# Optimization experiments

Hardware: AMD Instinct MI355X
Metric: run time of the kernel (lower is better)

Reference implementation:

```python
import jax, jax.numpy as jnp
import numpy as np
import math

D_MODEL, D_STATE, D_CONV = 1024, 16, 4
D_INNER = 2 * D_MODEL
DT_RANK = math.ceil(D_MODEL / 16)
B, L = 4, 2048


def setup_inputs() -> dict:
    key = jax.random.key(0)
    ks = jax.random.split(key, 10)
    s = 0.02
    x = jax.random.normal(ks[0], (B, L, D_MODEL), dtype=jnp.float32)
    ln_g = jnp.ones((D_MODEL,), jnp.float32)
    ln_b = jnp.zeros((D_MODEL,), jnp.float32)
    W_in = jax.random.normal(ks[1], (D_MODEL, 2 * D_INNER), jnp.float32) * s
    conv_w = jax.random.normal(ks[2], (D_INNER, 1, D_CONV), jnp.float32) * s
    conv_b = jnp.zeros((D_INNER,), jnp.float32)
    W_xp = jax.random.normal(ks[3], (D_INNER, DT_RANK + 2 * D_STATE), jnp.float32) * s
    W_dt = jax.random.normal(ks[4], (DT_RANK, D_INNER), jnp.float32) * (DT_RANK ** -0.5)
    # inverse-softplus of dt ~ 0.01 (between dt_min=0.001 and dt_max=0.1)
    dt_bias = jnp.full((D_INNER,), float(np.log(np.expm1(0.01))), jnp.float32)
    # S4D-real init: A = 1..d_state per channel
    A_log = jnp.log(jnp.broadcast_to(jnp.arange(1, D_STATE + 1, dtype=jnp.float32), (D_INNER, D_STATE)))
    D_skip = jnp.ones((D_INNER,), jnp.float32)
    W_out = jax.random.normal(ks[5], (D_INNER, D_MODEL), jnp.float32) * s
    return dict(x=x, ln_g=ln_g, ln_b=ln_b, W_in=W_in, conv_w=conv_w, conv_b=conv_b,
                W_xp=W_xp, W_dt=W_dt, dt_bias=dt_bias, A_log=A_log, D_skip=D_skip, W_out=W_out)


def _layernorm(x, g, b, eps=1e-5):
    m = jnp.mean(x, axis=-1, keepdims=True)
    v = jnp.mean(jnp.square(x - m), axis=-1, keepdims=True)
    return (x - m) * jax.lax.rsqrt(v + eps) * g + b


def _mamba(xn, W_in, conv_w, conv_b, W_xp, W_dt, dt_bias, A_log, D_skip, W_out):
    # xn: [B, L, d_model]
    xz = xn @ W_in                                   # [B, L, 2*d_inner]
    xi, z = jnp.split(xz, 2, axis=-1)                # each [B, L, d_inner]
    # depthwise causal conv over sequence
    xi_t = jnp.transpose(xi, (0, 2, 1))              # [B, d_inner, L]
    xc = jax.lax.conv_general_dilated(
        xi_t, conv_w, window_strides=(1,), padding=[(D_CONV - 1, 0)],
        feature_group_count=D_INNER, dimension_numbers=('NCH', 'OIH', 'NCH'))
    xc = jnp.transpose(xc, (0, 2, 1)) + conv_b       # [B, L, d_inner]
    xc = jax.nn.silu(xc)
    # input-dependent dt, B, C
    x_dbl = xc @ W_xp                                # [B, L, dt_rank + 2*d_state]
    dt_lo, Bm, Cm = jnp.split(x_dbl, [DT_RANK, DT_RANK + D_STATE], axis=-1)
    delta = jax.nn.softplus(dt_lo @ W_dt + dt_bias)  # [B, L, d_inner]
    A = -jnp.exp(A_log)                              # [d_inner, d_state]

    def step(h, inp):
        dt_t, B_t, C_t, u_t = inp                    # [B,D], [B,N], [B,N], [B,D]
        dA = jnp.exp(dt_t[..., None] * A)            # [B, D, N]
        h = h * dA + (dt_t * u_t)[..., None] * B_t[:, None, :]
        y = jnp.einsum('bdn,bn->bd', h, C_t)
        return h, y

    h0 = jnp.zeros((xn.shape[0], D_INNER, D_STATE), xn.dtype)
    inputs = (jnp.transpose(delta, (1, 0, 2)), jnp.transpose(Bm, (1, 0, 2)),
              jnp.transpose(Cm, (1, 0, 2)), jnp.transpose(xc, (1, 0, 2)))
    _, ys = jax.lax.scan(step, h0, inputs)           # ys: [L, B, d_inner]
    y = jnp.transpose(ys, (1, 0, 2)) + xc * D_skip   # [B, L, d_inner]
    y = y * jax.nn.silu(z)
    return y @ W_out                                 # [B, L, d_model]


def reference(x, ln_g, ln_b, W_in, conv_w, conv_b, W_xp, W_dt, dt_bias, A_log, D_skip, W_out):
    xn = _layernorm(x, ln_g, ln_b)
    return _mamba(xn, W_in, conv_w, conv_b, W_xp, W_dt, dt_bias, A_log, D_skip, W_out) + x
```

## Files before the change

### kernel.cpp

```cpp
#include <hip/hip_runtime.h>

#define DM 1024
#define DI 2048
#define DS 16
#define DTR 64
#define LL 2048
#define NROW 8192

typedef unsigned short u16;
typedef unsigned int u32;
typedef __bf16 bf16x8 __attribute__((ext_vector_type(8)));
typedef float f32x4 __attribute__((ext_vector_type(4)));
typedef float v2f __attribute__((ext_vector_type(2)));

__device__ __forceinline__ float bf2f(u16 u) {
  unsigned int v = ((unsigned int)u) << 16;
  return __builtin_bit_cast(float, v);
}
__device__ __forceinline__ u16 f2bf(float f) {
  unsigned int x = __builtin_bit_cast(unsigned int, f);
  x = x + 0x7fffu + ((x >> 16) & 1u);
  return (u16)(x >> 16);
}
__device__ __forceinline__ float lo_bf(u32 v) { return __builtin_bit_cast(float, v << 16); }
__device__ __forceinline__ float hi_bf(u32 v) { return __builtin_bit_cast(float, v & 0xFFFF0000u); }
__device__ __forceinline__ u32 pack_bf(float a, float b) {
  return (u32)f2bf(a) | ((u32)f2bf(b) << 16);
}
__device__ __forceinline__ bool io_f32(const u16* lng) { return lng[0] == 0; }

__device__ __forceinline__ void async16(const void* g, void* l) {
  __builtin_amdgcn_global_load_lds(
      (const __attribute__((address_space(1))) unsigned int*)g,
      (__attribute__((address_space(3))) unsigned int*)l, 16, 0, 0);
}

__device__ __forceinline__ void pow16v(float e1, v2f* E) {
  float e2 = e1 * e1;
  v2f sq = {e2, e2};
  E[0] = (v2f){e1, e2};
#pragma unroll
  for (int k = 1; k < 8; k++) E[k] = E[k - 1] * sq;
}

__device__ void transpose_dev(const void* __restrict__ in, u16* __restrict__ out,
                              int R, int C, int Cp, int bx, int by, bool f32,
                              int tid, u16 (*tile)[33]) {
  int c0 = bx * 32, r0 = by * 32;
  int tx = tid & 31, ty = tid >> 5;
#pragma unroll
  for (int i = 0; i < 4; i++) {
    int r = r0 + ty + i * 8, c = c0 + tx;
    u16 v = 0;
    if (r < R && c < C) {
      if (f32) v = f2bf(((const float*)in)[(size_t)r * C + c]);
      else     v = ((const u16*)in)[(size_t)r * C + c];
    }
    tile[ty + i * 8][tx] = v;
  }
  __syncthreads();
#pragma unroll
  for (int i = 0; i < 4; i++) {
    int oc = c0 + ty + i * 8, orr = r0 + tx;
    if (oc < Cp && orr < R) out[(size_t)oc * R + orr] = tile[tx][ty + i * 8];
  }
}

__global__ __launch_bounds__(256) void prep_k(
    const void* __restrict__ W_in, u16* __restrict__ W_inT,
    const void* __restrict__ W_dt, u16* __restrict__ W_dtT,
    const void* __restrict__ W_xp, u16* __restrict__ W_xpT,
    const void* __restrict__ W_out, u16* __restrict__ W_outT,
    const void* __restrict__ x, const u16* __restrict__ g,
    const u16* __restrict__ b, u16* __restrict__ xn) {
  __shared__ u16 tile[32][33];
  __shared__ float rs_[4], rq_[4];
  bool f32 = io_f32(g);
  int tid = threadIdx.x;
  int bid = blockIdx.x;
  if (bid < 4096) {
    transpose_dev(W_in, W_inT, 1024, 4096, 4096, bid & 127, bid >> 7, f32, tid, tile);
    return;
  } else if (bid < 4224) {
    bid -= 4096;
    transpose_dev(W_dt, W_dtT, 64, 2048, 2048, bid & 63, bid >> 6, f32, tid, tile);
    return;
  } else if (bid < 4480) {
    bid -= 4224;
    transpose_dev(W_xp, W_xpT, 2048, 96, 128, bid & 3, bid >> 2, f32, tid, tile);
    return;
  } else if (bid < 6528) {
    bid -= 4480;
    transpose_dev(W_out, W_outT, 2048, 1024, 1024, bid & 31, bid >> 5, f32, tid, tile);
    return;
  }
  int row = bid - 6528;
  float f[4];
  if (f32) {
    float4 v = ((const float4*)((const float*)x + (size_t)row * DM))[tid];
    f[0] = v.x; f[1] = v.y; f[2] = v.z; f[3] = v.w;
  } else {
    ushort4 v = ((const ushort4*)((const u16*)x + (size_t)row * DM))[tid];
    f[0] = bf2f(v.x); f[1] = bf2f(v.y); f[2] = bf2f(v.z); f[3] = bf2f(v.w);
  }
  float s = f[0] + f[1] + f[2] + f[3];
  float q = f[0] * f[0] + f[1] * f[1] + f[2] * f[2] + f[3] * f[3];
#pragma unroll
  for (int off = 32; off; off >>= 1) {
    s += __shfl_down(s, off, 64);
    q += __shfl_down(q, off, 64);
  }
  int wid = tid >> 6, lane = tid & 63;
  if (lane == 0) { rs_[wid] = s; rq_[wid] = q; }
  __syncthreads();
  float ts = rs_[0] + rs_[1] + rs_[2] + rs_[3];
  float tq = rq_[0] + rq_[1] + rq_[2] + rq_[3];
  float mean = ts * (1.f / DM);
  float var = tq * (1.f / DM) - mean * mean;
  float inv = rsqrtf(var + 1e-5f);
  int c = tid * 4;
  ushort4 o;
  u16* po = (u16*)&o;
#pragma unroll
  for (int k = 0; k < 4; k++) {
    float gk = f32 ? ((const float*)g)[c + k] : bf2f(g[c + k]);
    float bk = f32 ? ((const float*)b)[c + k] : bf2f(b[c + k]);
    po[k] = f2bf((f[k] - mean) * inv * gk + bk);
  }
  ((ushort4*)(xn + (size_t)row * DM))[tid] = o;
}

template <int EPI>
__device__ __forceinline__ void gemm_body(const u16* __restrict__ A,
                                          const u16* __restrict__ BT,
                                          void* __restrict__ C,
                                          const void* __restrict__ extra,
                                          int M, int N, int Klen, int ldk,
                                          const u16* __restrict__ lng, int mOff,
                                          u16* ldsA, u16* ldsB) {
  int tid = threadIdx.x;
  int wid = tid >> 6, lane = tid & 63;
  int l15 = lane & 15, quad = lane >> 4;
  int bm = blockIdx.x * 128;
  int bn;
  const u16* Ae = A;
  const u16* Be = BT;
  float* Cpart = nullptr;
  if (EPI == 5) {
    bn = 0;
    int ky = blockIdx.y;
    Ae += (size_t)ky * Klen;
    Be += (size_t)ky * Klen;
    Cpart = (float*)C + (size_t)ky * M * N;
  } else {
    bn = blockIdx.y * 128;
  }
  int wrow = (wid >> 1) * 64, wcol = (wid & 1) * 64;

  f32x4 zero = {0.f, 0.f, 0.f, 0.f};
  f32x4 acc[4][4];
#pragma unroll
  for (int i = 0; i < 4; i++)
#pragma unroll
    for (int j = 0; j < 4; j++) acc[i][j] = zero;

  int row0 = tid >> 2;
  int colb = (tid & 3) * 16;
  const char* Ap0 = (const char*)Ae + ((size_t)(bm + row0) * ldk) * 2 + colb;
  const char* Ap1 = (const char*)Ae + ((size_t)(bm + row0 + 64) * ldk) * 2 + colb;
  const char* Bp0 = (const char*)Be + ((size_t)(bn + row0) * ldk) * 2 + colb;
  const char* Bp1 = (const char*)Be + ((size_t)(bn + row0 + 64) * ldk) * 2 + colb;
  u16* la = ldsA + wid * 512;
  u16* lb = ldsB + wid * 512;

  for (int k0 = 0; k0 < Klen; k0 += 64) {
    size_t kb = (size_t)k0 * 2;
    async16(Ap0 + kb, la);
    async16(Ap1 + kb, la + 2048);
    async16(Ap0 + kb + 64, la + 4096);
    async16(Ap1 + kb + 64, la + 6144);
    async16(Bp0 + kb, lb);
    async16(Bp1 + kb, lb + 2048);
    async16(Bp0 + kb + 64, lb + 4096);
    async16(Bp1 + kb + 64, lb + 6144);
    __syncthreads();
#pragma unroll
    for (int s = 0; s < 2; s++) {
      bf16x8 af[4], bfr[4];
#pragma unroll
      for (int i = 0; i < 4; i++)
        af[i] = *(const bf16x8*)&ldsA[s * 4096 + (wrow + i * 16 + l15) * 32 + quad * 8];
#pragma unroll
      for (int j = 0; j < 4; j++)
        bfr[j] = *(const bf16x8*)&ldsB[s * 4096 + (wcol + j * 16 + l15) * 32 + quad * 8];
#pragma unroll
      for (int i = 0; i < 4; i++)
#pragma unroll
        for (int j = 0; j < 4; j++)
          acc[i][j] = __builtin_amdgcn_mfma_f32_16x16x32_bf16(af[i], bfr[j], acc[i][j], 0, 0, 0);
    }
    __syncthreads();
  }

  bool f32 = (EPI == 2 || EPI == 3) ? io_f32(lng) : false;
  if ((EPI == 2 || EPI == 3) && !f32) {
    u16* tile = ldsA;
#pragma unroll
    for (int i = 0; i < 4; i++) {
#pragma unroll
      for (int j = 0; j < 4; j++) {
        int gn = bn + wcol + j * 16 + l15;
#pragma unroll
        for (int r = 0; r < 4; r++) {
          int lr = wrow + i * 16 + quad * 4 + r;
          float v = acc[i][j][r];
          if (EPI == 2) {
            v += bf2f(((const u16*)extra)[gn]);
            v = (v > 20.f) ? v : log1pf(__expf(v));
          } else {
            v += bf2f(((const u16*)extra)[(size_t)(bm + lr + mOff) * N + gn]);
          }
          tile[lr * 128 + wcol + j * 16 + l15] = f2bf(v);
        }
      }
    }
    __syncthreads();
#pragma unroll
    for (int g = 0; g < 8; g++) {
      int gi = g * 256 + tid;
      int row = gi >> 4, cg = gi & 15;
      uint4 v4 = *(const uint4*)&tile[row * 128 + cg * 8];
      *(uint4*)((u16*)C + (size_t)(bm + row + mOff) * N + bn + cg * 8) = v4;
    }
    return;
  }
#pragma unroll
  for (int i = 0; i < 4; i++) {
#pragma unroll
    for (int j = 0; j < 4; j++) {
      int gn = bn + wcol + j * 16 + l15;
#pragma unroll
      for (int r = 0; r < 4; r++) {
        int gm = bm + wrow + i * 16 + quad * 4 + r;
        float v = acc[i][j][r];
        if (EPI == 2) {
          float bias = ((const float*)extra)[gn];
          v += bias;
          float sp = (v > 20.f) ? v : log1pf(__expf(v));
          ((u16*)C)[(size_t)gm * N + gn] = f2bf(sp);
        } else if (EPI == 3) {
          size_t idx = (size_t)(gm + mOff) * N + gn;
          v += ((const float*)extra)[idx];
          ((float*)C)[idx] = v;
        } else {
          Cpart[(size_t)gm * N + gn] = v;
        }
      }
    }
  }
}

#define GEMM_WRAP(name, EPI)                                                        \
  __global__ __launch_bounds__(256) void name(                                      \
      const u16* __restrict__ A, const u16* __restrict__ BT, void* __restrict__ C,  \
      const void* __restrict__ extra, int M, int N, int Klen, int ldk,              \
      const u16* __restrict__ lng, int mOff) {                                      \
    __shared__ __align__(16) u16 lds[16384];                                        \
    gemm_body<EPI>(A, BT, C, extra, M, N, Klen, ldk, lng, mOff, lds, lds + 8192);   \
  }

GEMM_WRAP(gemm_xp_k, 5)
GEMM_WRAP(gemm_dt_k, 2)
GEMM_WRAP(gemm_out_k, 3)

__global__ __launch_bounds__(512, 2) void gemm_in256_k(
    const u16* __restrict__ A, const u16* __restrict__ BT,
    u16* __restrict__ C, u16* __restrict__ Z, int ldk, int Klen) {
  __shared__ __align__(16) u16 lds[65536];
  const int tid = threadIdx.x;
  const int wid = tid >> 6, lane = tid & 63;
  const int l15 = lane & 15, quad = lane >> 4;
  const int bm = blockIdx.x * 256, bn = blockIdx.y * 256;
  const int wrow = (wid >> 2) * 128;
  const int wcol = (wid & 3) * 64;

  const int srow = tid >> 3;
  const int sg = ((tid & 7) ^ (srow & 7)) * 8;
  const u16* Ag[4];
  const u16* Bg[4];
#pragma unroll
  for (int s = 0; s < 4; s++) {
    Ag[s] = A + (size_t)(bm + s * 64 + srow) * ldk + sg;
    Bg[s] = BT + (size_t)(bn + s * 64 + srow) * ldk + sg;
  }
  const int sdst = wid * 512;

  int rA[2], rB[2];
#pragma unroll
  for (int ks = 0; ks < 2; ks++) {
    int gsw = ((ks * 4 + quad) ^ (l15 & 7)) * 8;
    rA[ks] = (wrow + l15) * 64 + gsw;
    rB[ks] = 16384 + (wcol + l15) * 64 + gsw;
  }

  f32x4 acc[8][4];
  f32x4 zero = {0.f, 0.f, 0.f, 0.f};
#pragma unroll
  for (int i = 0; i < 8; i++)
#pragma unroll
    for (int j = 0; j < 4; j++) acc[i][j] = zero;

  const int NT = Klen >> 6;
  async16(Ag[0], &lds[sdst]);
  async16(Ag[1], &lds[4096 + sdst]);
  async16(Ag[2], &lds[8192 + sdst]);
  async16(Ag[3], &lds[12288 + sdst]);
  async16(Bg[0], &lds[16384 + sdst]);
  async16(Bg[1], &lds[20480 + sdst]);
  async16(Bg[2], &lds[24576 + sdst]);
  async16(Bg[3], &lds[28672 + sdst]);
  if (NT > 1) {
    async16(Ag[0] + 64, &lds[32768 + sdst]);
    async16(Ag[1] + 64, &lds[36864 + sdst]);
    async16(Ag[2] + 64, &lds[40960 + sdst]);
    async16(Ag[3] + 64, &lds[45056 + sdst]);
    async16(Bg[0] + 64, &lds[49152 + sdst]);
    async16(Bg[1] + 64, &lds[53248 + sdst]);
    async16(Bg[2] + 64, &lds[57344 + sdst]);
    async16(Bg[3] + 64, &lds[61440 + sdst]);
  }
  asm volatile("s_waitcnt vmcnt(8)" ::: "memory");
  __builtin_amdgcn_s_barrier();
  __builtin_amdgcn_sched_barrier(0);

  bf16x8 aLo[4][2], aHi[4][2], b0[2][2], b1[2][2];
#pragma unroll
  for (int mf = 0; mf < 4; mf++) {
    aLo[mf][0] = *(const bf16x8*)&lds[rA[0] + mf * 1024];
    aLo[mf][1] = *(const bf16x8*)&lds[rA[1] + mf * 1024];
  }
#pragma unroll
  for (int nf = 0; nf < 2; nf++)
#pragma unroll
    for (int ks = 0; ks < 2; ks++) {
      b0[nf][ks] = *(const bf16x8*)&lds[rB[ks] + nf * 1024];
      b1[nf][ks] = *(const bf16x8*)&lds[rB[ks] + (2 + nf) * 1024];
    }

  for (int t = 0; t < NT; ++t) {
    const int bb = (t & 1) << 15;
    const int nb = bb ^ 32768;
    const int k2 = (t + 2) << 6;
    const bool st1 = (t + 1 < NT), st2 = (t + 2 < NT);

    __builtin_amdgcn_s_setprio(1);
#pragma unroll
    for (int ks = 0; ks < 2; ks++)
#pragma unroll
      for (int mf = 0; mf < 4; mf++)
#pragma unroll
        for (int nf = 0; nf < 2; nf++)
          acc[mf][nf] = __builtin_amdgcn_mfma_f32_16x16x32_bf16(aLo[mf][ks], b0[nf][ks], acc[mf][nf], 0, 0, 0);
    __builtin_amdgcn_s_setprio(0);
#pragma unroll
    for (int mf = 0; mf < 4; mf++) {
      aHi[mf][0] = *(const bf16x8*)&lds[bb + rA[0] + 4096 + mf * 1024];
      aHi[mf][1] = *(const bf16x8*)&lds[bb + rA[1] + 4096 + mf * 1024];
    }
    __builtin_amdgcn_s_setprio(1);
#pragma unroll
    for (int ks = 0; ks < 2; ks++)
#pragma unroll
      for (int mf = 0; mf < 4; mf++)
#pragma unroll
        for (int nf = 0; nf < 2; nf++)
          acc[mf][2 + nf] = __builtin_amdgcn_mfma_f32_16x16x32_bf16(aLo[mf][ks], b1[nf][ks], acc[mf][2 + nf], 0, 0, 0);
    __builtin_amdgcn_s_setprio(0);

    asm volatile("s_waitcnt lgkmcnt(0)" ::: "memory");
    __builtin_amdgcn_sched_barrier(0);
    asm volatile("s_waitcnt vmcnt(0)" ::: "memory");
    __builtin_amdgcn_s_barrier();
    __builtin_amdgcn_sched_barrier(0);

    if (st2) {
      async16(Ag[0] + k2, &lds[bb + sdst]);
      async16(Ag[1] + k2, &lds[bb + 4096 + sdst]);
      async16(Ag[2] + k2, &lds[bb + 8192 + sdst]);
      async16(Ag[3] + k2, &lds[bb + 12288 + sdst]);
      async16(Bg[0] + k2, &lds[bb + 16384 + sdst]);
      async16(Bg[1] + k2, &lds[bb + 20480 + sdst]);
      async16(Bg[2] + k2, &lds[bb + 24576 + sdst]);
      async16(Bg[3] + k2, &lds[bb + 28672 + sdst]);
    }
    if (st1) {
#pragma unroll
      for (int mf = 0; mf < 4; mf++) {
        aLo[mf][0] = *(const bf16x8*)&lds[nb + rA[0] + mf * 1024];
        aLo[mf][1] = *(const bf16x8*)&lds[nb + rA[1] + mf * 1024];
      }
    }
    __builtin_amdgcn_s_setprio(1);
#pragma unroll
    for (int ks = 0; ks < 2; ks++)
#pragma unroll
      for (int mf = 0; mf < 4; mf++)
#pragma unroll
        for (int nf = 0; nf < 2; nf++)
          acc[4 + mf][nf] = __builtin_amdgcn_mfma_f32_16x16x32_bf16(aHi[mf][ks], b0[nf][ks], acc[4 + mf][nf], 0, 0, 0);
    __builtin_amdgcn_s_setprio(0);
    if (st1) {
#pragma unroll
      for (int nf = 0; nf < 2; nf++)
#pragma unroll
        for (int ks = 0; ks < 2; ks++)
          b0[nf][ks] = *(const bf16x8*)&lds[nb + rB[ks] + nf * 1024];
    }
    __builtin_amdgcn_s_setprio(1);
#pragma unroll
    for (int ks = 0; ks < 2; ks++)
#pragma unroll
      for (int mf = 0; mf < 4; mf++)
#pragma unroll
        for (int nf = 0; nf < 2; nf++)
          acc[4 + mf][2 + nf] = __builtin_amdgcn_mfma_f32_16x16x32_bf16(aHi[mf][ks], b1[nf][ks], acc[4 + mf][2 + nf], 0, 0, 0);
    __builtin_amdgcn_s_setprio(0);
    if (st1) {
#pragma unroll
      for (int nf = 0; nf < 2; nf++)
#pragma unroll
        for (int ks = 0; ks < 2; ks++)
          b1[nf][ks] = *(const bf16x8*)&lds[nb + rB[ks] + (2 + nf) * 1024];
    }
  }

  __syncthreads();
  {
    const bool isZ = (bn >= DI);
#pragma unroll
    for (int i = 0; i < 8; i++) {
#pragma unroll
      for (int j = 0; j < 4; j++) {
        int lc = wcol + j * 16 + l15;
        int gr = lc >> 3, go = lc & 7;
#pragma unroll
        for (int r = 0; r < 4; r++) {
          int lr = wrow + i * 16 + quad * 4 + r;
          float v = acc[i][j][r];
          if (isZ) v = v / (1.f + __expf(-v));
          int grs = gr ^ ((lr & 7) ^ ((lr >> 3) & 7));
          lds[lr * 256 + grs * 8 + go] = f2bf(v);
        }
      }
    }
    __syncthreads();
    u16* outp = isZ ? (Z + (size_t)bm * DI + (bn - DI)) : (C + (size_t)bm * DI + bn);
#pragma unroll
    for (int g = 0; g < 16; g++) {
      int gi = g * 512 + tid;
      int row = gi >> 5, cg = gi & 31;
      int cgs = cg ^ ((row & 7) ^ ((row >> 3) & 7));
      uint4 v4 = *(const uint4*)&lds[row * 256 + cgs * 8];
      *(uint4*)(outp + (size_t)row * DI + cg * 8) = v4;
    }
  }
}

__global__ __launch_bounds__(256) void conv4_k(const u16* __restrict__ xi,
                                               const void* __restrict__ cw,
                                               const void* __restrict__ cb,
                                               u16* __restrict__ xc,
                                               const u16* __restrict__ lng) {
  bool f32 = io_f32(lng);
  int idx = blockIdx.x * 256 + threadIdx.x;
  int c = idx & (DI - 1);
  int rq = idx >> 11;
  int l4 = (rq & (LL / 4 - 1)) * 4;
  int b = rq >> 9;
  float w[4], bias;
  if (f32) {
    float4 w4 = *(const float4*)((const float*)cw + (size_t)c * 4);
    w[0] = w4.x; w[1] = w4.y; w[2] = w4.z; w[3] = w4.w;
    bias = ((const float*)cb)[c];
  } else {
    ushort4 w4 = *(const ushort4*)((const u16*)cw + (size_t)c * 4);
    w[0] = bf2f(w4.x); w[1] = bf2f(w4.y); w[2] = bf2f(w4.z); w[3] = bf2f(w4.w);
    bias = bf2f(((const u16*)cb)[c]);
  }
  size_t base = ((size_t)(b * LL + l4)) * DI + c;
  float v[7];
#pragma unroll
  for (int j = 0; j < 7; j++) {
    int lj = l4 - 3 + j;
    v[j] = (lj >= 0) ? bf2f(xi[base + (size_t)(j - 3) * DI]) : 0.f;
  }
#pragma unroll
  for (int r = 0; r < 4; r++) {
    float acc = bias + v[r] * w[0] + v[r + 1] * w[1] + v[r + 2] * w[2] + v[r + 3] * w[3];
    float sv = acc / (1.f + __expf(-acc));
    xc[base + (size_t)r * DI] = f2bf(sv);
  }
}

__global__ __launch_bounds__(256) void reduce_dtlo_k(const float* __restrict__ Cpart,
                                                     float* __restrict__ xdbl,
                                                     u16* __restrict__ dtlo, int M) {
  int i = blockIdx.x * 256 + threadIdx.x;
  size_t MN = (size_t)M * 128;
  float v = Cpart[i] + Cpart[MN + i] + Cpart[2 * MN + i] + Cpart[3 * MN + i];
  xdbl[i] = v;
  int j = i & 127, m = i >> 7;
  if (j < 64) dtlo[(size_t)m * 64 + j] = f2bf(v);
}

__device__ __forceinline__ bool fastA(const void* A_log, bool f32, int d0) {
  bool fast = true;
#pragma unroll
  for (int c = 0; c < 2; c++)
    for (int n = 0; n < 16; n++) {
      float al = f32 ? ((const float*)A_log)[(d0 + c) * DS + n]
                     : bf2f(((const u16*)A_log)[(d0 + c) * DS + n]);
      float Av = __expf(al);
      fast = fast && (__builtin_fabsf(Av - (float)(n + 1)) <= 1e-3f * (n + 1));
    }
  return fast;
}

template <int S>
__global__ __launch_bounds__(256) void scan_p1(const u16* __restrict__ delta,
                                               const u16* __restrict__ xc,
                                               const float* __restrict__ xdbl,
                                               const void* __restrict__ A_log,
                                               const u16* __restrict__ lng,
                                               float* __restrict__ Pbuf,
                                               float* __restrict__ Lbuf,
                                               float* __restrict__ sumbuf,
                                               int NS) {
  bool f32 = io_f32(lng);
  int tid = threadIdx.x;
  int seg = blockIdx.x, dch = blockIdx.y, bL = blockIdx.z;
  int d0 = (dch * 256 + tid) * 2;
  size_t rb = (size_t)bL * LL;
  int l0 = seg * S;
  extern __shared__ float bc[];
#pragma unroll 2
  for (int i = tid; i < S * 4; i += 256) {
    int t = i >> 2, k = (i & 3) * 4;
    *(float4*)&bc[t * 16 + k] = *(const float4*)&xdbl[(rb + l0 + t) * 128 + 64 + k];
  }
  __syncthreads();
  size_t sb = ((((size_t)bL * NS + seg) * DI) + d0) * DS;
  const u32* dpu = (const u32*)(delta + (rb + l0) * DI + d0);
  const u32* upu = (const u32*)(xc + (rb + l0) * DI + d0);
  if (fastA(A_log, f32, d0)) {
    v2f h0[8], h1[8];
#pragma unroll
    for (int k = 0; k < 8; k++) { h0[k] = (v2f){0.f, 0.f}; h1[k] = (v2f){0.f, 0.f}; }
    float sum0 = 0.f, sum1 = 0.f;
    const int T = 8;
    for (int t0 = 0; t0 < S; t0 += T) {
      u32 dv[T], uv[T];
#pragma unroll
      for (int j = 0; j < T; j++) {
        dv[j] = dpu[j * (DI / 2)];
        uv[j] = upu[j * (DI / 2)];
      }
      dpu += T * (DI / 2);
      upu += T * (DI / 2);
#pragma unroll
      for (int j = 0; j < T; j++) {
        float dt0 = lo_bf(dv[j]), dt1 = hi_bf(dv[j]);
        float u0 = lo_bf(uv[j]), u1 = hi_bf(uv[j]);
        sum0 += dt0; sum1 += dt1;
        const v2f* B2 = (const v2f*)&bc[(t0 + j) * 16];
        v2f E[8];
        pow16v(__expf(-dt0), E);
        float com0 = dt0 * u0;
        v2f cv0 = {com0, com0};
#pragma unroll
        for (int k = 0; k < 8; k++) h0[k] = h0[k] * E[k] + B2[k] * cv0;
        pow16v(__expf(-dt1), E);
        float com1 = dt1 * u1;
        v2f cv1 = {com1, com1};
#pragma unroll
        for (int k = 0; k < 8; k++) h1[k] = h1[k] * E[k] + B2[k] * cv1;
      }
    }
#pragma unroll
    for (int k = 0; k < 8; k++) { *(v2f*)&Lbuf[sb + 2 * k] = h0[k]; *(v2f*)&Lbuf[sb + 16 + 2 * k] = h1[k]; }
    if (sumbuf) {
      *(v2f*)&sumbuf[((size_t)(bL * NS + seg)) * DI + d0] = (v2f){sum0, sum1};
    } else {
      v2f P[8];
      pow16v(__expf(-sum0), P);
#pragma unroll
      for (int k = 0; k < 8; k++) *(v2f*)&Pbuf[sb + 2 * k] = P[k];
      pow16v(__expf(-sum1), P);
#pragma unroll
      for (int k = 0; k < 8; k++) *(v2f*)&Pbuf[sb + 16 + 2 * k] = P[k];
    }
  } else {
    for (int c = 0; c < 2; c++) {
      int d = d0 + c;
      float A2[16], h[16], P[16];
#pragma unroll
      for (int n = 0; n < 16; n++) {
        float al = f32 ? ((const float*)A_log)[d * DS + n] : bf2f(((const u16*)A_log)[d * DS + n]);
        A2[n] = -__expf(al);
        h[n] = 0.f; P[n] = 1.f;
      }
      const u16* dp = delta + (rb + l0) * DI + d;
      const u16* up = xc + (rb + l0) * DI + d;
      for (int t = 0; t < S; t++) {
        float dt = bf2f(dp[(size_t)t * DI]);
        float u = bf2f(up[(size_t)t * DI]);
        float com = dt * u;
        const float* Bf = &bc[t * 16];
#pragma unroll
        for (int n = 0; n < 16; n++) {
          float dA = __expf(dt * A2[n]);
          h[n] = fmaf(h[n], dA, com * Bf[n]);
          P[n] *= dA;
        }
      }
#pragma unroll
      for (int n = 0; n < 16; n++) { Pbuf[sb + 16 * c + n] = P[n]; Lbuf[sb + 16 * c + n] = h[n]; }
    }
  }
}

__global__ __launch_bounds__(256) void scan_p2(float* __restrict__ Pbuf,
                                               float* __restrict__ Lbuf,
                                               const float* __restrict__ sumbuf,
                                               const void* __restrict__ A_log,
                                               const u16* __restrict__ lng, int NS) {
  int idx = blockIdx.x * 256 + threadIdx.x;
  int bL = idx >> 15;
  int dn = idx & 32767;
  int d = dn >> 4, n = dn & 15;
  bool useSum = false;
  if (sumbuf) {
    bool f32 = io_f32(lng);
    useSum = fastA(A_log, f32, d & ~1);
  }
  float np1 = (float)(n + 1);
  float H = 0.f;
  for (int s = 0; s < NS; s++) {
    size_t o = ((size_t)(bL * NS + s) << 15) + dn;
    float Lv = Lbuf[o];
    float P = useSum ? __expf(-sumbuf[((size_t)(bL * NS + s)) * DI + d] * np1)
                     : Pbuf[o];
    Lbuf[o] = H;
    H = fmaf(P, H, Lv);
  }
}

template <int S>
__global__ __launch_bounds__(256) void scan_p3(u16* __restrict__ dy,
                                               const u16* __restrict__ xc,
                                               const float* __restrict__ xdbl,
                                               const u16* __restrict__ z,
                                               const void* __restrict__ A_log,
                                               const void* __restrict__ D_skip,
                                               const u16* __restrict__ lng,
                                               const float* __restrict__ Lbuf,
                                               int NS) {
  bool f32 = io_f32(lng);
  int tid = threadIdx.x;
  int seg = blockIdx.x, dch = blockIdx.y, bL = blockIdx.z;
  int d0 = (dch * 256 + tid) * 2;
  size_t rb = (size_t)bL * LL;
  int l0 = seg * S;
  extern __shared__ float bc[];
#pragma unroll 2
  for (int i = tid; i < S * 8; i += 256) {
    int t = i >> 3, k = (i & 7) * 4;
    *(float4*)&bc[t * 32 + k] = *(const float4*)&xdbl[(rb + l0 + t) * 128 + 64 + k];
  }
  __syncthreads();
  size_t sb = ((((size_t)bL * NS + seg) * DI) + d0) * DS;
  float Dv0 = f32 ? ((const float*)D_skip)[d0] : bf2f(((const u16*)D_skip)[d0]);
  float Dv1 = f32 ? ((const float*)D_skip)[d0 + 1] : bf2f(((const u16*)D_skip)[d0 + 1]);
  u32* dpu = (u32*)(dy + (rb + l0) * DI + d0);
  const u32* upu = (const u32*)(xc + (rb + l0) * DI + d0);
  const u32* zpu = (const u32*)(z + (rb + l0) * DI + d0);
  if (fastA(A_log, f32, d0)) {
    v2f h0[8], h1[8];
#pragma unroll
    for (int k = 0; k < 8; k++) {
      h0[k] = *(const v2f*)&Lbuf[sb + 2 * k];
      h1[k] = *(const v2f*)&Lbuf[sb + 16 + 2 * k];
    }
    const int T = 8;
    for (int t0 = 0; t0 < S; t0 += T) {
      u32 dv[T], uv[T], zv[T];
#pragma unroll
      for (int j = 0; j < T; j++) {
        dv[j] = dpu[j * (DI / 2)];
        uv[j] = upu[j * (DI / 2)];
        zv[j] = zpu[j * (DI / 2)];
      }
      upu += T * (DI / 2);
      zpu += T * (DI / 2);
#pragma unroll
      for (int j = 0; j < T; j++) {
        float dt0 = lo_bf(dv[j]), dt1 = hi_bf(dv[j]);
        float u0 = lo_bf(uv[j]), u1 = hi_bf(uv[j]);
        float zg0 = lo_bf(zv[j]), zg1 = hi_bf(zv[j]);
        const v2f* B2 = (const v2f*)&bc[(t0 + j) * 32];
        const v2f* C2 = (const v2f*)&bc[(t0 + j) * 32 + 16];
        v2f E[8];
        pow16v(__expf(-dt0), E);
        float com0 = dt0 * u0;
        v2f cv = {com0, com0};
        v2f a0 = {0.f, 0.f}, a1 = {0.f, 0.f};
#pragma unroll
        for (int k = 0; k < 8; k += 2) {
          h0[k] = h0[k] * E[k] + B2[k] * cv;
          h0[k + 1] = h0[k + 1] * E[k + 1] + B2[k + 1] * cv;
          a0 += h0[k] * C2[k];
          a1 += h0[k + 1] * C2[k + 1];
        }
        float cs0 = (a0.x + a0.y) + (a1.x + a1.y);
        pow16v(__expf(-dt1), E);
        float com1 = dt1 * u1;
        cv = (v2f){com1, com1};
        a0 = (v2f){0.f, 0.f}; a1 = (v2f){0.f, 0.f};
#pragma unroll
        for (int k = 0; k < 8; k += 2) {
          h1[k] = h1[k] * E[k] + B2[k] * cv;
          h1[k + 1] = h1[k + 1] * E[k + 1] + B2[k + 1] * cv;
          a0 += h1[k] * C2[k];
          a1 += h1[k + 1] * C2[k + 1];
        }
        float cs1 = (a0.x + a0.y) + (a1.x + a1.y);
        float y0 = (cs0 + u0 * Dv0) * zg0;
        float y1 = (cs1 + u1 * Dv1) * zg1;
        dpu[j * (DI / 2)] = pack_bf(y0, y1);
      }
      dpu += T * (DI / 2);
    }
  } else {
    for (int c = 0; c < 2; c++) {
      int d = d0 + c;
      float A2[16], h[16];
#pragma unroll
      for (int n = 0; n < 16; n++) {
        float al = f32 ? ((const float*)A_log)[d * DS + n] : bf2f(((const u16*)A_log)[d * DS + n]);
        A2[n] = -__expf(al);
        h[n] = Lbuf[sb + 16 * c + n];
      }
      float Dv = (c == 0) ? Dv0 : Dv1;
      u16* dp = dy + (rb + l0) * DI + d;
      const u16* up = xc + (rb + l0) * DI + d;
      const u16* zp = z + (rb + l0) * DI + d;
      for (int t = 0; t < S; t++) {
        float dt = bf2f(dp[(size_t)t * DI]);
        float u = bf2f(up[(size_t)t * DI]);
        float zg = bf2f(zp[(size_t)t * DI]);
        float com = dt * u;
        const float* Bf = &bc[t * 32];
        const float* Cf = &bc[t * 32 + 16];
        float cs = 0.f;
#pragma unroll
        for (int n = 0; n < 16; n++) {
          float dA = __expf(dt * A2[n]);
          h[n] = fmaf(h[n], dA, com * Bf[n]);
          cs = fmaf(h[n], Cf[n], cs);
        }
        dp[(size_t)t * DI] = f2bf((cs + u * Dv) * zg);
      }
    }
  }
}

static void launch_scan(int NS, int nb, u16* xi, u16* xc, float* xdbl, u16* z,
                        const u16* A_log, const u16* D_sk, const u16* ln_g,
                        float* Pbuf, float* Lbuf, float* sumbuf,
                        hipStream_t stream) {
  int S = LL / NS;
  dim3 g1(NS, 4, nb);
  if (S == 32) {
    scan_p1<32><<<g1, 256, 32 * 64, stream>>>(xi, xc, xdbl, A_log, ln_g, Pbuf, Lbuf, sumbuf, NS);
  } else if (S == 64) {
    scan_p1<64><<<g1, 256, 64 * 64, stream>>>(xi, xc, xdbl, A_log, ln_g, Pbuf, Lbuf, sumbuf, NS);
  } else {
    scan_p1<128><<<g1, 256, 128 * 64, stream>>>(xi, xc, xdbl, A_log, ln_g, Pbuf, Lbuf, sumbuf, NS);
  }
  scan_p2<<<nb * 128, 256, 0, stream>>>(Pbuf, Lbuf, sumbuf, A_log, ln_g, NS);
  if (S == 32) {
    scan_p3<32><<<g1, 256, 32 * 128, stream>>>(xi, xc, xdbl, z, A_log, D_sk, ln_g, Lbuf, NS);
  } else if (S == 64) {
    scan_p3<64><<<g1, 256, 64 * 128, stream>>>(xi, xc, xdbl, z, A_log, D_sk, ln_g, Lbuf, NS);
  } else {
    scan_p3<128><<<g1, 256, 128 * 128, stream>>>(xi, xc, xdbl, z, A_log, D_sk, ln_g, Lbuf, NS);
  }
}

extern "C" void kernel_launch(void* const* d_in, const int* in_sizes, int n_in,
                              void* d_out, int out_size, void* d_ws, size_t ws_size,
                              hipStream_t stream) {
  const u16* x = (const u16*)d_in[0];
  const u16* ln_g = (const u16*)d_in[1];
  const u16* ln_b = (const u16*)d_in[2];
  const u16* W_in = (const u16*)d_in[3];
  const u16* cw = (const u16*)d_in[4];
  const u16* cb = (const u16*)d_in[5];
  const u16* W_xp = (const u16*)d_in[6];
  const u16* W_dt = (const u16*)d_in[7];
  const u16* dt_b = (const u16*)d_in[8];
  const u16* A_log = (const u16*)d_in[9];
  const u16* D_sk = (const u16*)d_in[10];
  const u16* W_out = (const u16*)d_in[11];

  char* ws = (char*)d_ws;
  const size_t MB = 1024 * 1024;

  if (ws_size >= 124 * MB) {
    int NS = (ws_size >= 180 * MB) ? 64 : (ws_size >= 144 * MB) ? 32 : 16;
    u16* xc = (u16*)(ws + 0);
    u16* xn = xc;
    u16* W_inT = (u16*)(ws + 16 * MB);
    u16* xi = (u16*)(ws + 32 * MB);
    u16* z = (u16*)(ws + 64 * MB);
    float* xdbl = (float*)(ws + 96 * MB);
    u16* dtlo = (u16*)(ws + 100 * MB);
    u16* W_xpT = (u16*)(ws + 101 * MB);
    u16* W_dtT = (u16*)(ws + 102 * MB);
    u16* W_outT = (u16*)(ws + 103 * MB);
    size_t stateSz = (size_t)NS * 4 * DI * DS * 4;
    float* Cpart = (float*)(ws + 107 * MB);
    float* Pbuf = (float*)(ws + 107 * MB);
    float* Lbuf = (float*)(ws + 107 * MB + stateSz);
    float* sumbuf = (NS >= 32) ? (float*)(ws + 107 * MB + 2 * stateSz) : nullptr;

    prep_k<<<6528 + NROW, 256, 0, stream>>>(W_in, W_inT, W_dt, W_dtT, W_xp, W_xpT,
                                            W_out, W_outT, x, ln_g, ln_b, xn);
    gemm_in256_k<<<dim3(NROW / 256, (2 * DI) / 256), 512, 0, stream>>>(xn, W_inT, xi, z, DM, DM);
    conv4_k<<<(NROW / 4 * DI) / 256, 256, 0, stream>>>(xi, cw, cb, xc, ln_g);
    gemm_xp_k<<<dim3(64, 4), 256, 0, stream>>>(xc, W_xpT, Cpart, nullptr, NROW, 128, 512, DI, ln_g, 0);
    reduce_dtlo_k<<<(NROW * 128) / 256, 256, 0, stream>>>(Cpart, xdbl, dtlo, NROW);
    gemm_dt_k<<<dim3(64, 16), 256, 0, stream>>>(dtlo, W_dtT, xi, dt_b, NROW, DI, DTR, DTR, ln_g, 0);
    launch_scan(NS, 4, xi, xc, xdbl, z, A_log, D_sk, ln_g, Pbuf, Lbuf, sumbuf, stream);
    gemm_out_k<<<dim3(64, 8), 256, 0, stream>>>(xi, W_outT, d_out, x, NROW, DM, DI, DI, ln_g, 0);
  } else {
    int NS = 32;
    u16* W_inT = (u16*)(ws + 0);
    u16* W_xpT = (u16*)(ws + 8 * MB);
    u16* W_dtT = (u16*)(ws + 9 * MB);
    u16* W_outT = (u16*)(ws + 10 * MB);
    u16* xn = (u16*)(ws + 14 * MB);
    u16* xi = (u16*)(ws + 30 * MB);
    u16* z = (u16*)(ws + 38 * MB);
    u16* xc = (u16*)(ws + 46 * MB);
    float* xdbl = (float*)(ws + 54 * MB);
    u16* dtlo = (u16*)(ws + 55 * MB);
    float* Cpart = (float*)(ws + 56 * MB);
    float* Pbuf = (float*)(ws + 56 * MB);
    float* Lbuf = (float*)(ws + 61 * MB);

    prep_k<<<6528 + NROW, 256, 0, stream>>>(W_in, W_inT, W_dt, W_dtT, W_xp, W_xpT,
                                            W_out, W_outT, x, ln_g, ln_b, xn);
    for (int b = 0; b < 4; b++) {
      const u16* xnb = xn + (size_t)b * LL * DM;
      gemm_in256_k<<<dim3(LL / 256, (2 * DI) / 256), 512, 0, stream>>>(xnb, W_inT, xi, z, DM, DM);
      conv4_k<<<(LL / 4 * DI) / 256, 256, 0, stream>>>(xi, cw, cb, xc, ln_g);
      gemm_xp_k<<<dim3(16, 4), 256, 0, stream>>>(xc, W_xpT, Cpart, nullptr, LL, 128, 512, DI, ln_g, 0);
      reduce_dtlo_k<<<(LL * 128) / 256, 256, 0, stream>>>(Cpart, xdbl, dtlo, LL);
      gemm_dt_k<<<dim3(16, 16), 256, 0, stream>>>(dtlo, W_dtT, xi, dt_b, LL, DI, DTR, DTR, ln_g, 0);
      launch_scan(NS, 1, xi, xc, xdbl, z, A_log, D_sk, ln_g, Pbuf, Lbuf, nullptr, stream);
      gemm_out_k<<<dim3(16, 8), 256, 0, stream>>>(xi, W_outT, d_out, x, LL, DM, DI, DI, ln_g, b * LL);
    }
  }
}
```

Baseline: 492.6 us.

## Replace output GEMM with 256x128 pipelined kernel and vectorize depthwise conv

Swaps the generic 128x128 output-projection GEMM for a dedicated 512-thread kernel. It uses 256x128 tiles, double-buffered async global-to-LDS loads, swizzled LDS and interleaved MFMA with LDS reads, plus a swizzled bf16 epilogue that adds the residual. The conv kernel now handles 8 channels per thread with 16-byte loads and stores instead of scalar bf16 accesses. The aim is better operand reuse and overlap in the output GEMM and fewer memory transactions in the conv. In exchange, the GEMM uses more LDS and registers per block and gets fewer blocks (256 instead of 512) on the large path.

```diff
diff --git a/kernel.cpp b/kernel.cpp
--- a/kernel.cpp
+++ b/kernel.cpp
@@ -202,8 +202,8 @@
     __syncthreads();
   }
 
-  bool f32 = (EPI == 2 || EPI == 3) ? io_f32(lng) : false;
-  if ((EPI == 2 || EPI == 3) && !f32) {
+  bool f32 = (EPI == 2) ? io_f32(lng) : false;
+  if (EPI == 2 && !f32) {
     u16* tile = ldsA;
 #pragma unroll
     for (int i = 0; i < 4; i++) {
@@ -214,12 +214,8 @@
         for (int r = 0; r < 4; r++) {
           int lr = wrow + i * 16 + quad * 4 + r;
           float v = acc[i][j][r];
-          if (EPI == 2) {
-            v += bf2f(((const u16*)extra)[gn]);
-            v = (v > 20.f) ? v : log1pf(__expf(v));
-          } else {
-            v += bf2f(((const u16*)extra)[(size_t)(bm + lr + mOff) * N + gn]);
-          }
+          v += bf2f(((const u16*)extra)[gn]);
+          v = (v > 20.f) ? v : log1pf(__expf(v));
           tile[lr * 128 + wcol + j * 16 + l15] = f2bf(v);
         }
       }
@@ -248,10 +244,6 @@
           v += bias;
           float sp = (v > 20.f) ? v : log1pf(__expf(v));
           ((u16*)C)[(size_t)gm * N + gn] = f2bf(sp);
-        } else if (EPI == 3) {
-          size_t idx = (size_t)(gm + mOff) * N + gn;
-          v += ((const float*)extra)[idx];
-          ((float*)C)[idx] = v;
         } else {
           Cpart[(size_t)gm * N + gn] = v;
         }
@@ -271,7 +263,6 @@
 
 GEMM_WRAP(gemm_xp_k, 5)
 GEMM_WRAP(gemm_dt_k, 2)
-GEMM_WRAP(gemm_out_k, 3)
 
 __global__ __launch_bounds__(512, 2) void gemm_in256_k(
     const u16* __restrict__ A, const u16* __restrict__ BT,
@@ -466,6 +457,190 @@
   }
 }
 
+__global__ __launch_bounds__(512, 2) void gemm_out256_k(
+    const u16* __restrict__ A, const u16* __restrict__ BT,
+    void* __restrict__ C, const void* __restrict__ extra,
+    int N, int ldk, int Klen, const u16* __restrict__ lng, int mOff) {
+  __shared__ __align__(16) u16 lds[49152];
+  const int tid = threadIdx.x;
+  const int wid = tid >> 6, lane = tid & 63;
+  const int l15 = lane & 15, quad = lane >> 4;
+  const int bm = blockIdx.x * 256, bn = blockIdx.y * 128;
+  const int wrow = (wid >> 2) * 128;
+  const int wcol = (wid & 3) * 32;
+
+  const int srow = tid >> 3;
+  const int sg = ((tid & 7) ^ (srow & 7)) * 8;
+  const u16* Ag[4];
+  const u16* Bg[2];
+#pragma unroll
+  for (int s = 0; s < 4; s++) Ag[s] = A + (size_t)(bm + s * 64 + srow) * ldk + sg;
+#pragma unroll
+  for (int s = 0; s < 2; s++) Bg[s] = BT + (size_t)(bn + s * 64 + srow) * ldk + sg;
+  const int sdst = wid * 512;
+
+  int rA[2], rB[2];
+#pragma unroll
+  for (int ks = 0; ks < 2; ks++) {
+    int gsw = ((ks * 4 + quad) ^ (l15 & 7)) * 8;
+    rA[ks] = (wrow + l15) * 64 + gsw;
+    rB[ks] = 16384 + (wcol + l15) * 64 + gsw;
+  }
+
+  f32x4 acc[8][2];
+  f32x4 zero = {0.f, 0.f, 0.f, 0.f};
+#pragma unroll
+  for (int i = 0; i < 8; i++)
+#pragma unroll
+    for (int j = 0; j < 2; j++) acc[i][j] = zero;
+
+  const int NT = Klen >> 6;
+  async16(Ag[0], &lds[sdst]);
+  async16(Ag[1], &lds[4096 + sdst]);
+  async16(Ag[2], &lds[8192 + sdst]);
+  async16(Ag[3], &lds[12288 + sdst]);
+  async16(Bg[0], &lds[16384 + sdst]);
+  async16(Bg[1], &lds[20480 + sdst]);
+  if (NT > 1) {
+    async16(Ag[0] + 64, &lds[24576 + sdst]);
+    async16(Ag[1] + 64, &lds[24576 + 4096 + sdst]);
+    async16(Ag[2] + 64, &lds[24576 + 8192 + sdst]);
+    async16(Ag[3] + 64, &lds[24576 + 12288 + sdst]);
+    async16(Bg[0] + 64, &lds[24576 + 16384 + sdst]);
+    async16(Bg[1] + 64, &lds[24576 + 20480 + sdst]);
+  }
+  asm volatile("s_waitcnt vmcnt(6)" ::: "memory");
+  __builtin_amdgcn_s_barrier();
+  __builtin_amdgcn_sched_barrier(0);
+
+  bf16x8 aLo[4][2], aHi[4][2], b0[2], b1[2];
+#pragma unroll
+  for (int mf = 0; mf < 4; mf++) {
+    aLo[mf][0] = *(const bf16x8*)&lds[rA[0] + mf * 1024];
+    aLo[mf][1] = *(const bf16x8*)&lds[rA[1] + mf * 1024];
+  }
+#pragma unroll
+  for (int ks = 0; ks < 2; ks++) {
+    b0[ks] = *(const bf16x8*)&lds[rB[ks]];
+    b1[ks] = *(const bf16x8*)&lds[rB[ks] + 1024];
+  }
+
+  for (int t = 0; t < NT; ++t) {
+    const int bb = (t & 1) * 24576;
+    const int nb = bb ^ 24576;
+    const int k2 = (t + 2) << 6;
+    const bool st1 = (t + 1 < NT), st2 = (t + 2 < NT);
+
+    __builtin_amdgcn_s_setprio(1);
+#pragma unroll
+    for (int ks = 0; ks < 2; ks++)
+#pragma unroll
+      for (int mf = 0; mf < 4; mf++)
+        acc[mf][0] = __builtin_amdgcn_mfma_f32_16x16x32_bf16(aLo[mf][ks], b0[ks], acc[mf][0], 0, 0, 0);
+    __builtin_amdgcn_s_setprio(0);
+#pragma unroll
+    for (int mf = 0; mf < 4; mf++) {
+      aHi[mf][0] = *(const bf16x8*)&lds[bb + rA[0] + 4096 + mf * 1024];
+      aHi[mf][1] = *(const bf16x8*)&lds[bb + rA[1] + 4096 + mf * 1024];
+    }
+    __builtin_amdgcn_s_setprio(1);
+#pragma unroll
+    for (int ks = 0; ks < 2; ks++)
+#pragma unroll
+      for (int mf = 0; mf < 4; mf++)
+        acc[mf][1] = __builtin_amdgcn_mfma_f32_16x16x32_bf16(aLo[mf][ks], b1[ks], acc[mf][1], 0, 0, 0);
+    __builtin_amdgcn_s_setprio(0);
+
+    asm volatile("s_waitcnt lgkmcnt(0)" ::: "memory");
+    __builtin_amdgcn_sched_barrier(0);
+    asm volatile("s_waitcnt vmcnt(0)" ::: "memory");
+    __builtin_amdgcn_s_barrier();
+    __builtin_amdgcn_sched_barrier(0);
+
+    if (st2) {
+      async16(Ag[0] + k2, &lds[bb + sdst]);
+      async16(Ag[1] + k2, &lds[bb + 4096 + sdst]);
+      async16(Ag[2] + k2, &lds[bb + 8192 + sdst]);
+      async16(Ag[3] + k2, &lds[bb + 12288 + sdst]);
+      async16(Bg[0] + k2, &lds[bb + 16384 + sdst]);
+      async16(Bg[1] + k2, &lds[bb + 20480 + sdst]);
+    }
+    if (st1) {
+#pragma unroll
+      for (int mf = 0; mf < 4; mf++) {
+        aLo[mf][0] = *(const bf16x8*)&lds[nb + rA[0] + mf * 1024];
+        aLo[mf][1] = *(const bf16x8*)&lds[nb + rA[1] + mf * 1024];
+      }
+    }
+    __builtin_amdgcn_s_setprio(1);
+#pragma unroll
+    for (int ks = 0; ks < 2; ks++)
+#pragma unroll
+      for (int mf = 0; mf < 4; mf++)
+        acc[4 + mf][0] = __builtin_amdgcn_mfma_f32_16x16x32_bf16(aHi[mf][ks], b0[ks], acc[4 + mf][0], 0, 0, 0);
+    __builtin_amdgcn_s_setprio(0);
+    if (st1) {
+#pragma unroll
+      for (int ks = 0; ks < 2; ks++) b0[ks] = *(const bf16x8*)&lds[nb + rB[ks]];
+    }
+    __builtin_amdgcn_s_setprio(1);
+#pragma unroll
+    for (int ks = 0; ks < 2; ks++)
+#pragma unroll
+      for (int mf = 0; mf < 4; mf++)
+        acc[4 + mf][1] = __builtin_amdgcn_mfma_f32_16x16x32_bf16(aHi[mf][ks], b1[ks], acc[4 + mf][1], 0, 0, 0);
+    __builtin_amdgcn_s_setprio(0);
+    if (st1) {
+#pragma unroll
+      for (int ks = 0; ks < 2; ks++) b1[ks] = *(const bf16x8*)&lds[nb + rB[ks] + 1024];
+    }
+  }
+
+  bool f32 = io_f32(lng);
+  __syncthreads();
+  if (!f32) {
+#pragma unroll
+    for (int i = 0; i < 8; i++) {
+#pragma unroll
+      for (int j = 0; j < 2; j++) {
+        int lc = wcol + j * 16 + l15;
+        int gr = lc >> 3, go = lc & 7;
+#pragma unroll
+        for (int r = 0; r < 4; r++) {
+          int lr = wrow + i * 16 + quad * 4 + r;
+          float v = acc[i][j][r];
+          v += bf2f(((const u16*)extra)[(size_t)(bm + lr + mOff) * N + bn + lc]);
+          int grs = gr ^ ((lr & 7) ^ ((lr >> 3) & 7));
+          lds[lr * 128 + grs * 8 + go] = f2bf(v);
+        }
+      }
+    }
+    __syncthreads();
+#pragma unroll
+    for (int g = 0; g < 8; g++) {
+      int gi = g * 512 + tid;
+      int row = gi >> 4, cg = gi & 15;
+      int cgs = cg ^ ((row & 7) ^ ((row >> 3) & 7));
+      uint4 v4 = *(const uint4*)&lds[row * 128 + cgs * 8];
+      *(uint4*)((u16*)C + (size_t)(bm + row + mOff) * N + bn + cg * 8) = v4;
+    }
+  } else {
+#pragma unroll
+    for (int i = 0; i < 8; i++) {
+#pragma unroll
+      for (int j = 0; j < 2; j++) {
+        int gn = bn + wcol + j * 16 + l15;
+#pragma unroll
+        for (int r = 0; r < 4; r++) {
+          int gm = bm + wrow + i * 16 + quad * 4 + r;
+          size_t idx = (size_t)(gm + mOff) * N + gn;
+          ((float*)C)[idx] = acc[i][j][r] + ((const float*)extra)[idx];
+        }
+      }
+    }
+  }
+}
+
 __global__ __launch_bounds__(256) void conv4_k(const u16* __restrict__ xi,
                                                const void* __restrict__ cw,
                                                const void* __restrict__ cb,
@@ -473,32 +648,58 @@
                                                const u16* __restrict__ lng) {
   bool f32 = io_f32(lng);
   int idx = blockIdx.x * 256 + threadIdx.x;
-  int c = idx & (DI - 1);
-  int rq = idx >> 11;
+  int c8 = (idx & (DI / 8 - 1)) * 8;
+  int rq = idx >> 8;
   int l4 = (rq & (LL / 4 - 1)) * 4;
   int b = rq >> 9;
-  float w[4], bias;
-  if (f32) {
-    float4 w4 = *(const float4*)((const float*)cw + (size_t)c * 4);
-    w[0] = w4.x; w[1] = w4.y; w[2] = w4.z; w[3] = w4.w;
-    bias = ((const float*)cb)[c];
-  } else {
-    ushort4 w4 = *(const ushort4*)((const u16*)cw + (size_t)c * 4);
-    w[0] = bf2f(w4.x); w[1] = bf2f(w4.y); w[2] = bf2f(w4.z); w[3] = bf2f(w4.w);
-    bias = bf2f(((const u16*)cb)[c]);
-  }
-  size_t base = ((size_t)(b * LL + l4)) * DI + c;
-  float v[7];
+  float w[8][4], bi[8];
+#pragma unroll
+  for (int e = 0; e < 8; e++) {
+    if (f32) {
+      float4 w4 = ((const float4*)cw)[c8 + e];
+      w[e][0] = w4.x; w[e][1] = w4.y; w[e][2] = w4.z; w[e][3] = w4.w;
+      bi[e] = ((const float*)cb)[c8 + e];
+    } else {
+      ushort4 w4 = ((const ushort4*)cw)[c8 + e];
+      w[e][0] = bf2f(w4.x); w[e][1] = bf2f(w4.y); w[e][2] = bf2f(w4.z); w[e][3] = bf2f(w4.w);
+      bi[e] = bf2f(((const u16*)cb)[c8 + e]);
+    }
+  }
+  size_t base = ((size_t)(b * LL + l4)) * DI + c8;
+  float v[7][8];
 #pragma unroll
   for (int j = 0; j < 7; j++) {
     int lj = l4 - 3 + j;
-    v[j] = (lj >= 0) ? bf2f(xi[base + (size_t)(j - 3) * DI]) : 0.f;
+    if (lj >= 0) {
+      uint4 q = *(const uint4*)&xi[base + (size_t)(j - 3) * DI];
+      u32 qq[4] = {q.x, q.y, q.z, q.w};
+#pragma unroll
+      for (int e = 0; e < 4; e++) {
+        v[j][2 * e] = lo_bf(qq[e]);
+        v[j][2 * e + 1] = hi_bf(qq[e]);
+      }
+    } else {
+#pragma unroll
+      for (int e = 0; e < 8; e++) v[j][e] = 0.f;
+    }
   }
 #pragma unroll
   for (int r = 0; r < 4; r++) {
-    float acc = bias + v[r] * w[0] + v[r + 1] * w[1] + v[r + 2] * w[2] + v[r + 3] * w[3];
-    float sv = acc / (1.f + __expf(-acc));
-    xc[base + (size_t)r * DI] = f2bf(sv);
+    u32 out[4];
+#pragma unroll
+    for (int e = 0; e < 8; e += 2) {
+      float a0 = bi[e], a1 = bi[e + 1];
+#pragma unroll
+      for (int k = 0; k < 4; k++) {
+        a0 += v[r + k][e] * w[e][k];
+        a1 += v[r + k][e + 1] * w[e + 1][k];
+      }
+      a0 = a0 / (1.f + __expf(-a0));
+      a1 = a1 / (1.f + __expf(-a1));
+      out[e >> 1] = pack_bf(a0, a1);
+    }
+    uint4 o4 = {out[0], out[1], out[2], out[3]};
+    *(uint4*)&xc[base + (size_t)r * DI] = o4;
   }
 }
 
@@ -837,12 +1038,12 @@
     prep_k<<<6528 + NROW, 256, 0, stream>>>(W_in, W_inT, W_dt, W_dtT, W_xp, W_xpT,
                                             W_out, W_outT, x, ln_g, ln_b, xn);
     gemm_in256_k<<<dim3(NROW / 256, (2 * DI) / 256), 512, 0, stream>>>(xn, W_inT, xi, z, DM, DM);
-    conv4_k<<<(NROW / 4 * DI) / 256, 256, 0, stream>>>(xi, cw, cb, xc, ln_g);
+    conv4_k<<<(NROW / 4) * (DI / 8) / 256, 256, 0, stream>>>(xi, cw, cb, xc, ln_g);
     gemm_xp_k<<<dim3(64, 4), 256, 0, stream>>>(xc, W_xpT, Cpart, nullptr, NROW, 128, 512, DI, ln_g, 0);
     reduce_dtlo_k<<<(NROW * 128) / 256, 256, 0, stream>>>(Cpart, xdbl, dtlo, NROW);
     gemm_dt_k<<<dim3(64, 16), 256, 0, stream>>>(dtlo, W_dtT, xi, dt_b, NROW, DI, DTR, DTR, ln_g, 0);
     launch_scan(NS, 4, xi, xc, xdbl, z, A_log, D_sk, ln_g, Pbuf, Lbuf, sumbuf, stream);
-    gemm_out_k<<<dim3(64, 8), 256, 0, stream>>>(xi, W_outT, d_out, x, NROW, DM, DI, DI, ln_g, 0);
+    gemm_out256_k<<<dim3(NROW / 256, DM / 128), 512, 0, stream>>>(xi, W_outT, d_out, x, DM, DI, DI, ln_g, 0);
   } else {
     int NS = 32;
     u16* W_inT = (u16*)(ws + 0);
@@ -864,12 +1065,12 @@
     for (int b = 0; b < 4; b++) {
       const u16* xnb = xn + (size_t)b * LL * DM;
       gemm_in256_k<<<dim3(LL / 256, (2 * DI) / 256), 512, 0, stream>>>(xnb, W_inT, xi, z, DM, DM);
-      conv4_k<<<(LL / 4 * DI) / 256, 256, 0, stream>>>(xi, cw, cb, xc, ln_g);
+      conv4_k<<<(LL / 4) * (DI / 8) / 256, 256, 0, stream>>>(xi, cw, cb, xc, ln_g);
       gemm_xp_k<<<dim3(16, 4), 256, 0, stream>>>(xc, W_xpT, Cpart, nullptr, LL, 128, 512, DI, ln_g, 0);
       reduce_dtlo_k<<<(LL * 128) / 256, 256, 0, stream>>>(Cpart, xdbl, dtlo, LL);
       gemm_dt_k<<<dim3(16, 16), 256, 0, stream>>>(dtlo, W_dtT, xi, dt_b, LL, DI, DTR, DTR, ln_g, 0);
       launch_scan(NS, 1, xi, xc, xdbl, z, A_log, D_sk, ln_g, Pbuf, Lbuf, nullptr, stream);
-      gemm_out_k<<<dim3(16, 8), 256, 0, stream>>>(xi, W_outT, d_out, x, LL, DM, DI, DI, ln_g, b * LL);
-    }
-  }
-}
+      gemm_out256_k<<<dim3(LL / 256, DM / 128), 512, 0, stream>>>(xi, W_outT, d_out, x, DM, DI, DI, ln_g, b * LL);
+    }
+  }
+}
```

Result: no change. 486.6 us (-1.2%).
